# Kernel optimization log

Measured on AMD Instinct MI355X. Metric: run time of the kernel, lower is better.

The kernel has to match this reference:

```python
import jax, jax.numpy as jnp
import numpy as np

N = 100_000      # nodes
E = 1_600_000    # edges (avg degree 16)
F_IN = 128       # in_feats
H = 128          # n_hidden
H2 = 64          # n_hidden // 2


def setup_inputs() -> dict:
    key = jax.random.key(0)
    k1, k2, k3, k4, k5 = jax.random.split(key, 5)
    features = jax.random.normal(k1, (N, F_IN), dtype=jnp.float32)
    W1 = jax.random.normal(k2, (F_IN, H), dtype=jnp.float32) * 0.05
    W2 = jax.random.normal(k3, (H, H2), dtype=jnp.float32) * 0.05
    src = jax.random.randint(k4, (E,), 0, N, dtype=jnp.int32)
    dst = jax.random.randint(k5, (E,), 0, N, dtype=jnp.int32)
    return {"features": features, "W1": W1, "W2": W2, "src": src, "dst": dst}


def _graph_conv(h, W, src, dst, out_norm, in_norm):
    # DGL GraphConv, norm='both', bias=False:
    #   rst = D_dst^{-1/2} * (A @ (D_src^{-1/2} * h)) @ W
    # (weight applied before/after aggregation is mathematically identical)
    h = h * out_norm[:, None]                                   # scale source feats
    agg = jax.ops.segment_sum(h[src], dst, num_segments=N)      # SpMM: sum over in-edges
    return (agg * in_norm[:, None]) @ W


def reference(features, W1, W2, src, dst):
    ones = jnp.ones(src.shape[0], dtype=jnp.float32)
    # allow_zero_in_degree=True -> DGL clamps degrees to min 1 for norm
    out_deg = jnp.clip(jax.ops.segment_sum(ones, src, num_segments=N), 1.0)
    in_deg = jnp.clip(jax.ops.segment_sum(ones, dst, num_segments=N), 1.0)
    out_norm = out_deg ** -0.5
    in_norm = in_deg ** -0.5
    h = _graph_conv(features, W1, src, dst, out_norm, in_norm)  # [N, H]
    h = jax.nn.relu(h)
    return _graph_conv(h, W2, src, dst, out_norm, in_norm)      # [N, H2]
```

## Files before the change

kernel.cpp:

```cpp
#include <hip/hip_runtime.h>
#include <cstdint>
#include <cstddef>

#define NN 100000
#define NE 1600000
#define FD 128
#define HD2 64

#define BSH 7
#define BSZ 128
#define NB ((NN + BSZ - 1) / BSZ)
#define TILE 4096
#define NTILE ((NE + TILE - 1) / TILE)
#define CAPB 2560

static_assert(NB <= 1024, "single-block bucket scan assumes <=1024 buckets");

typedef short bf16x8_t __attribute__((ext_vector_type(8)));
typedef float f32x4_t __attribute__((ext_vector_type(4)));

static __device__ __forceinline__ uint f2bf(float x) {
  uint u = __float_as_uint(x);
  return (u + 0x7fffu + ((u >> 16) & 1u)) >> 16;
}
static __device__ __forceinline__ uint pack2(float lo, float hi) {
  return f2bf(lo) | (f2bf(hi) << 16);
}
static __device__ __forceinline__ float bflo(uint v) { return __uint_as_float(v << 16); }
static __device__ __forceinline__ float bfhi(uint v) { return __uint_as_float(v & 0xffff0000u); }

__global__ void k_bucket(const int* __restrict__ src, const int* __restrict__ dst,
                         int* __restrict__ bcnt_d, int* __restrict__ bcnt_s,
                         uint* __restrict__ brec_d, ushort* __restrict__ brec_s) {
  __shared__ int hd[NB], gbd[NB], hs[NB], gbs[NB];
  for (int i = threadIdx.x; i < NB; i += 256) { hd[i] = 0; hs[i] = 0; }
  __syncthreads();
  int base = blockIdx.x * TILE;
  for (int i = threadIdx.x; i < TILE; i += 256) {
    int e = base + i;
    if (e < NE) {
      atomicAdd(&hd[dst[e] >> BSH], 1);
      atomicAdd(&hs[src[e] >> BSH], 1);
    }
  }
  __syncthreads();
  for (int i = threadIdx.x; i < NB; i += 256) {
    int cd = hd[i], cs = hs[i];
    gbd[i] = cd ? atomicAdd(bcnt_d + i, cd) : 0;
    gbs[i] = cs ? atomicAdd(bcnt_s + i, cs) : 0;
    hd[i] = 0;
    hs[i] = 0;
  }
  __syncthreads();
  for (int i = threadIdx.x; i < TILE; i += 256) {
    int e = base + i;
    if (e < NE) {
      int d = dst[e], sv = src[e];
      int bd = d >> BSH, bs = sv >> BSH;
      int rd = gbd[bd] + atomicAdd(&hd[bd], 1);
      if (rd < CAPB)
        brec_d[(size_t)bd * CAPB + rd] = ((uint)(d & (BSZ - 1)) << 17) | (uint)sv;
      int rs = gbs[bs] + atomicAdd(&hs[bs], 1);
      if (rs < CAPB)
        brec_s[(size_t)bs * CAPB + rs] = (ushort)(sv & (BSZ - 1));
    }
  }
}

__global__ __launch_bounds__(1024) void k_bscan(const int* __restrict__ bcnt_d,
                                                int* __restrict__ boff_d) {
  __shared__ int s[1024];
  int t = threadIdx.x;
  int v = (t < NB) ? bcnt_d[t] : 0;
  s[t] = v;
  __syncthreads();
#pragma unroll
  for (int off = 1; off < 1024; off <<= 1) {
    int x = (t >= off) ? s[t - off] : 0;
    __syncthreads();
    s[t] += x;
    __syncthreads();
  }
  if (t < NB) boff_d[t + 1] = s[t];
  if (t == 0) boff_d[0] = 0;
}

__global__ __launch_bounds__(256) void k_build(const uint* __restrict__ brec_d,
                                               const ushort* __restrict__ brec_s,
                                               const int* __restrict__ bcnt_d,
                                               const int* __restrict__ bcnt_s,
                                               const int* __restrict__ boff,
                                               int* __restrict__ row_ptr,
                                               float* __restrict__ in_norm,
                                               float* __restrict__ out_norm,
                                               int* __restrict__ csr) {
  __shared__ int lcnt[BSZ];
  __shared__ int lscan[BSZ + 1];
  __shared__ int lcur[BSZ];
  __shared__ int lcsr[CAPB];
  const int t = threadIdx.x;
  const int b = blockIdx.x;
  const int d0 = b * BSZ;
  const int nd = min(BSZ, NN - d0);
  const size_t rbase = (size_t)b * CAPB;

  const int len = min(bcnt_d[b], CAPB);
  const int ebase = boff[b];
  for (int i = t; i < BSZ; i += 256) lcnt[i] = 0;
  __syncthreads();
  for (int e = t; e < len; e += 256)
    atomicAdd(&lcnt[brec_d[rbase + e] >> 17], 1);
  __syncthreads();
  for (int i = t; i < nd; i += 256)
    in_norm[d0 + i] = rsqrtf((float)max(lcnt[i], 1));

  if (t < BSZ) lcur[t] = lcnt[t];
  __syncthreads();
#pragma unroll
  for (int off = 1; off < BSZ; off <<= 1) {
    int x = (t >= off && t < BSZ) ? lcur[t - off] : 0;
    __syncthreads();
    if (t < BSZ) lcur[t] += x;
    __syncthreads();
  }
  if (t < BSZ) lscan[t + 1] = lcur[t];
  if (t == 0) lscan[0] = 0;
  __syncthreads();
  for (int i = t; i <= nd; i += 256) row_ptr[d0 + i] = ebase + lscan[i];
  if (t < BSZ) lcur[t] = lscan[t];
  __syncthreads();

  for (int e = t; e < len; e += 256) {
    uint r = brec_d[rbase + e];
    int p = atomicAdd(&lcur[r >> 17], 1);
    lcsr[p] = (int)(r & 0x1FFFFu);
  }
  __syncthreads();
  for (int ld = t; ld < nd; ld += 256) {
    int a = lscan[ld], bnd = lscan[ld + 1];
    for (int i = a + 1; i < bnd; ++i) {
      int v = lcsr[i];
      int j = i - 1;
      while (j >= a && lcsr[j] > v) { lcsr[j + 1] = lcsr[j]; --j; }
      lcsr[j + 1] = v;
    }
  }
  __syncthreads();
  for (int i = t; i < len; i += 256) csr[ebase + i] = lcsr[i];

  __syncthreads();
  for (int i = t; i < BSZ; i += 256) lcnt[i] = 0;
  __syncthreads();
  const int len_s = min(bcnt_s[b], CAPB);
  for (int e = t; e < len_s; e += 256)
    atomicAdd(&lcnt[brec_s[rbase + e]], 1);
  __syncthreads();
  for (int i = t; i < nd; i += 256)
    out_norm[d0 + i] = rsqrtf((float)max(lcnt[i], 1));
}

__global__ void k_prep(const float* __restrict__ feat, const float* __restrict__ onorm,
                       uint* __restrict__ Xb,
                       const float* __restrict__ W1, const float* __restrict__ W2,
                       uint* __restrict__ W1t, uint* __restrict__ W2t) {
  int t = blockIdx.x * 256 + threadIdx.x;
  if (t < NN * 64) {
    int row = t >> 6, j = t & 63;
    float2 f = *(const float2*)(feat + (size_t)row * FD + 2 * j);
    float w = onorm[row];
    Xb[t] = pack2(f.x * w, f.y * w);
  } else {
    int i = t - NN * 64;
    if (i < FD * 64) {
      int n = i >> 6, kk = i & 63;
      W1t[i] = pack2(W1[(size_t)(2 * kk) * FD + n], W1[(size_t)(2 * kk + 1) * FD + n]);
    } else {
      int i2 = i - FD * 64;
      int n = i2 >> 6, kk = i2 & 63;
      W2t[i2] = pack2(W2[(size_t)(2 * kk) * HD2 + n], W2[(size_t)(2 * kk + 1) * HD2 + n]);
    }
  }
}

__global__ void k_spmm1b(const uint* __restrict__ Xb, const int* __restrict__ row_ptr,
                         const int* __restrict__ csr_src, const float* __restrict__ in_norm,
                         uint* __restrict__ Hb1) {
  int gid = blockIdx.x * blockDim.x + threadIdx.x;
  int row = gid >> 6;
  if (row >= NN) return;
  int lane = threadIdx.x & 63;
  int grp = lane >> 4;
  int gl = lane & 15;
  int e0 = row_ptr[row], e1 = row_ptr[row + 1];
  float2 a0 = {0.f, 0.f}, a1 = {0.f, 0.f}, a2 = {0.f, 0.f}, a3 = {0.f, 0.f};
#define ACC1(v)                                  \
  a0.x += bflo((v).x); a0.y += bfhi((v).x);      \
  a1.x += bflo((v).y); a1.y += bfhi((v).y);      \
  a2.x += bflo((v).z); a2.y += bfhi((v).z);      \
  a3.x += bflo((v).w); a3.y += bfhi((v).w);
  int e = e0;
  for (; e + 16 <= e1; e += 16) {
    int s0 = csr_src[e + grp];
    int s1 = csr_src[e + 4 + grp];
    int s2 = csr_src[e + 8 + grp];
    int s3 = csr_src[e + 12 + grp];
    uint4 v0 = *(const uint4*)(Xb + ((size_t)s0 << 6) + (gl << 2));
    uint4 v1 = *(const uint4*)(Xb + ((size_t)s1 << 6) + (gl << 2));
    uint4 v2 = *(const uint4*)(Xb + ((size_t)s2 << 6) + (gl << 2));
    uint4 v3 = *(const uint4*)(Xb + ((size_t)s3 << 6) + (gl << 2));
    ACC1(v0);
    ACC1(v1);
    ACC1(v2);
    ACC1(v3);
  }
  for (; e + 4 <= e1; e += 4) {
    int s0 = csr_src[e + grp];
    uint4 v0 = *(const uint4*)(Xb + ((size_t)s0 << 6) + (gl << 2));
    ACC1(v0);
  }
  if (e + grp < e1) {
    int s0 = csr_src[e + grp];
    uint4 v0 = *(const uint4*)(Xb + ((size_t)s0 << 6) + (gl << 2));
    ACC1(v0);
  }
#undef ACC1
#pragma unroll
  for (int m = 16; m <= 32; m <<= 1) {
    a0.x += __shfl_xor(a0.x, m); a0.y += __shfl_xor(a0.y, m);
    a1.x += __shfl_xor(a1.x, m); a1.y += __shfl_xor(a1.y, m);
    a2.x += __shfl_xor(a2.x, m); a2.y += __shfl_xor(a2.y, m);
    a3.x += __shfl_xor(a3.x, m); a3.y += __shfl_xor(a3.y, m);
  }
  if (grp == 0) {
    float wi = in_norm[row];
    uint4 o;
    o.x = pack2(a0.x * wi, a0.y * wi);
    o.y = pack2(a1.x * wi, a1.y * wi);
    o.z = pack2(a2.x * wi, a2.y * wi);
    o.w = pack2(a3.x * wi, a3.y * wi);
    *(uint4*)(Hb1 + ((size_t)row << 6) + (gl << 2)) = o;
  }
}

__global__ __launch_bounds__(256) void k_mlp(const uint* __restrict__ Hb1,
                                             const uint* __restrict__ W1t,
                                             const uint* __restrict__ W2t,
                                             const float* __restrict__ onorm,
                                             ushort* __restrict__ Tb) {
  __shared__ ushort h_lds[64 * FD];
  char* const lds = (char*)h_lds;
  const int tid = threadIdx.x;
  const int wid = tid >> 6;
  const int lane = tid & 63;
  const int l15 = lane & 15;
  const int g = lane >> 4;
  const int rowbase = blockIdx.x * 64 + wid * 16;

  const int ar = min(rowbase + l15, NN - 1);
  const uint* Arow = Hb1 + (size_t)ar * 64;
  bf16x8_t afr[4];
#pragma unroll
  for (int kc = 0; kc < 4; ++kc)
    afr[kc] = *(const bf16x8_t*)(Arow + kc * 16 + g * 4);

  float wnorm[4];
#pragma unroll
  for (int r = 0; r < 4; ++r)
    wnorm[r] = onorm[min(rowbase + 4 * g + r, NN - 1)];

#pragma unroll
  for (int nf = 0; nf < 8; ++nf) {
    f32x4_t acc = {0.f, 0.f, 0.f, 0.f};
#pragma unroll
    for (int kc = 0; kc < 4; ++kc) {
      bf16x8_t b = *(const bf16x8_t*)(W1t + (size_t)(nf * 16 + l15) * 64 + kc * 16 + g * 4);
      acc = __builtin_amdgcn_mfma_f32_16x16x32_bf16(afr[kc], b, acc, 0, 0, 0);
    }
#pragma unroll
    for (int r = 0; r < 4; ++r) {
      float hv = fmaxf(acc[r], 0.f) * wnorm[r];
      int row = wid * 16 + 4 * g + r;
      int byte = row * 256 + (nf * 16 + l15) * 2;
      byte ^= (row & 7) << 4;
      *(ushort*)(lds + byte) = (ushort)f2bf(hv);
    }
  }
  __syncthreads();

  bf16x8_t a2[4];
#pragma unroll
  for (int kc = 0; kc < 4; ++kc) {
    int row = wid * 16 + l15;
    int byte = row * 256 + (kc * 32 + 8 * g) * 2;
    byte ^= (row & 7) << 4;
    a2[kc] = *(const bf16x8_t*)(lds + byte);
  }
#pragma unroll
  for (int nf = 0; nf < 4; ++nf) {
    f32x4_t acc = {0.f, 0.f, 0.f, 0.f};
#pragma unroll
    for (int kc = 0; kc < 4; ++kc) {
      bf16x8_t b = *(const bf16x8_t*)(W2t + (size_t)(nf * 16 + l15) * 64 + kc * 16 + g * 4);
      acc = __builtin_amdgcn_mfma_f32_16x16x32_bf16(a2[kc], b, acc, 0, 0, 0);
    }
#pragma unroll
    for (int r = 0; r < 4; ++r) {
      int row = rowbase + 4 * g + r;
      if (row < NN)
        Tb[(size_t)row * HD2 + nf * 16 + l15] = (ushort)f2bf(acc[r]);
    }
  }
}

__global__ void k_spmm2b(const uint* __restrict__ Tb, const int* __restrict__ row_ptr,
                         const int* __restrict__ csr_src, const float* __restrict__ in_norm,
                         float* __restrict__ out) {
  int gid = blockIdx.x * blockDim.x + threadIdx.x;
  int row = gid >> 6;
  if (row >= NN) return;
  int lane = threadIdx.x & 63;
  int grp = lane >> 4;
  int gl = lane & 15;
  int e0 = row_ptr[row], e1 = row_ptr[row + 1];
  float2 a0 = {0.f, 0.f}, a1 = {0.f, 0.f};
#define ACC2(v)                                  \
  a0.x += bflo((v).x); a0.y += bfhi((v).x);      \
  a1.x += bflo((v).y); a1.y += bfhi((v).y);
  int e = e0;
  for (; e + 16 <= e1; e += 16) {
    int s0 = csr_src[e + grp];
    int s1 = csr_src[e + 4 + grp];
    int s2 = csr_src[e + 8 + grp];
    int s3 = csr_src[e + 12 + grp];
    uint2 v0 = *(const uint2*)(Tb + ((size_t)s0 << 5) + (gl << 1));
    uint2 v1 = *(const uint2*)(Tb + ((size_t)s1 << 5) + (gl << 1));
    uint2 v2 = *(const uint2*)(Tb + ((size_t)s2 << 5) + (gl << 1));
    uint2 v3 = *(const uint2*)(Tb + ((size_t)s3 << 5) + (gl << 1));
    ACC2(v0);
    ACC2(v1);
    ACC2(v2);
    ACC2(v3);
  }
  for (; e + 4 <= e1; e += 4) {
    int s0 = csr_src[e + grp];
    uint2 v0 = *(const uint2*)(Tb + ((size_t)s0 << 5) + (gl << 1));
    ACC2(v0);
  }
  if (e + grp < e1) {
    int s0 = csr_src[e + grp];
    uint2 v0 = *(const uint2*)(Tb + ((size_t)s0 << 5) + (gl << 1));
    ACC2(v0);
  }
#undef ACC2
#pragma unroll
  for (int m = 16; m <= 32; m <<= 1) {
    a0.x += __shfl_xor(a0.x, m); a0.y += __shfl_xor(a0.y, m);
    a1.x += __shfl_xor(a1.x, m); a1.y += __shfl_xor(a1.y, m);
  }
  if (grp == 0) {
    float wi = in_norm[row];
    *(float4*)(out + (size_t)row * HD2 + gl * 4) =
        make_float4(a0.x * wi, a0.y * wi, a1.x * wi, a1.y * wi);
  }
}

extern "C" void kernel_launch(void* const* d_in, const int* in_sizes, int n_in,
                              void* d_out, int out_size, void* d_ws, size_t ws_size,
                              hipStream_t stream) {
  const float* feat = (const float*)d_in[0];
  const float* W1   = (const float*)d_in[1];
  const float* W2   = (const float*)d_in[2];
  const int*   src  = (const int*)d_in[3];
  const int*   dst  = (const int*)d_in[4];
  float* out = (float*)d_out;

  char* p = (char*)d_ws;
  auto take = [&p](size_t bytes) -> char* {
    char* r = p;
    p += (bytes + 511) & ~(size_t)511;
    return r;
  };
  int*   row_ptr  = (int*)take((size_t)(NN + 1) * 4);
  int*   bcnt     = (int*)take((size_t)2 * NB * 4);
  int*   boff_d   = (int*)take((size_t)(NB + 1) * 4);
  float* out_norm = (float*)take((size_t)NN * 4);
  float* in_norm  = (float*)take((size_t)NN * 4);
  int*   csr_src  = (int*)take((size_t)NE * 4);
  uint*  W1t      = (uint*)take((size_t)FD * 64 * 4);
  uint*  W2t      = (uint*)take((size_t)HD2 * 64 * 4);
  uint*  Xb       = (uint*)take((size_t)NN * 64 * 4);
  uint*  Hb1      = (uint*)take((size_t)NN * 64 * 4);
  int*   bcnt_d   = bcnt;
  int*   bcnt_s   = bcnt + NB;
  ushort* Tb      = (ushort*)Xb;
  uint*   brec_d  = (uint*)Hb1;
  ushort* brec_s  = (ushort*)(Hb1 + (size_t)NB * CAPB);

  hipMemsetAsync(bcnt, 0, (size_t)2 * NB * 4, stream);

  k_bucket<<<NTILE, 256, 0, stream>>>(src, dst, bcnt_d, bcnt_s, brec_d, brec_s);
  k_bscan <<<1, 1024, 0, stream>>>(bcnt_d, boff_d);
  k_build <<<NB, 256, 0, stream>>>(brec_d, brec_s, bcnt_d, bcnt_s, boff_d,
                                   row_ptr, in_norm, out_norm, csr_src);
  k_prep  <<<(NN * 64 + FD * 64 + HD2 * 64) / 256, 256, 0, stream>>>(feat, out_norm, Xb,
                                                                     W1, W2, W1t, W2t);

  k_spmm1b<<<(NN * 64) / 256, 256, 0, stream>>>(Xb, row_ptr, csr_src, in_norm, Hb1);
  k_mlp   <<<(NN + 63) / 64, 256, 0, stream>>>(Hb1, W1t, W2t, out_norm, Tb);
  k_spmm2b<<<(NN * 64) / 256, 256, 0, stream>>>((const uint*)Tb, row_ptr, csr_src, in_norm, out);
}
```

Measured before the change: 276.2 us.

## Fuse feature prep into bucketing kernel and pack source norm into CSR entries

The feature-to-bf16 conversion and weight transposes now run as extra blocks of the bucketing kernel, and out-degree norms are computed in a new kernel alongside the bucket scan. Because X is no longer pre-scaled by out_norm, k_build encodes a compressed out_norm value into the upper 15 bits of each CSR entry next to the 17-bit source index, and SpMM1 decodes it and applies it as an FMA weight. This removes a separate prep launch and its dependency on out_norm. In exchange, the norm is quantized to a truncated float, which adds small precision error, and the bucketing tile size is also doubled.

Result: faster. 266.7 us (-3.4%).

```diff
diff --git a/kernel.cpp b/kernel.cpp
--- a/kernel.cpp
+++ b/kernel.cpp
@@ -10,11 +10,12 @@
 #define BSH 7
 #define BSZ 128
 #define NB ((NN + BSZ - 1) / BSZ)
-#define TILE 4096
+#define TILE 8192
 #define NTILE ((NE + TILE - 1) / TILE)
 #define CAPB 2560
-
-static_assert(NB <= 1024, "single-block bucket scan assumes <=1024 buckets");
+#define NPREP ((NN * 64 + FD * 64 + HD2 * 64 + 255) / 256)
+
+static_assert(NB <= 1024, "bucket scan assumes <=1024 buckets");
 
 typedef short bf16x8_t __attribute__((ext_vector_type(8)));
 typedef float f32x4_t __attribute__((ext_vector_type(4)));
@@ -29,13 +30,39 @@
 static __device__ __forceinline__ float bflo(uint v) { return __uint_as_float(v << 16); }
 static __device__ __forceinline__ float bfhi(uint v) { return __uint_as_float(v & 0xffff0000u); }
 
-__global__ void k_bucket(const int* __restrict__ src, const int* __restrict__ dst,
-                         int* __restrict__ bcnt_d, int* __restrict__ bcnt_s,
-                         uint* __restrict__ brec_d, ushort* __restrict__ brec_s) {
+static __device__ __forceinline__ float dec_w(uint r) {
+  return __uint_as_float(((r >> 17) + 0x38000u) << 12);
+}
+
+__global__ void k_bucket_prep(const int* __restrict__ src, const int* __restrict__ dst,
+                              int* __restrict__ bcnt_d, int* __restrict__ bcnt_s,
+                              uint* __restrict__ brec_d, ushort* __restrict__ brec_s,
+                              const float* __restrict__ feat, uint* __restrict__ Xraw,
+                              const float* __restrict__ W1, const float* __restrict__ W2,
+                              uint* __restrict__ W1t, uint* __restrict__ W2t) {
   __shared__ int hd[NB], gbd[NB], hs[NB], gbs[NB];
+  const int bid = blockIdx.x;
+  if (bid >= NTILE) {
+    int i = (bid - NTILE) * 256 + threadIdx.x;
+    if (i < NN * 64) {
+      float2 f = *(const float2*)(feat + 2 * (size_t)i);
+      Xraw[i] = pack2(f.x, f.y);
+    } else {
+      int j = i - NN * 64;
+      if (j < FD * 64) {
+        int n = j >> 6, kk = j & 63;
+        W1t[j] = pack2(W1[(size_t)(2 * kk) * FD + n], W1[(size_t)(2 * kk + 1) * FD + n]);
+      } else if (j < FD * 64 + HD2 * 64) {
+        int j2 = j - FD * 64;
+        int n = j2 >> 6, kk = j2 & 63;
+        W2t[j2] = pack2(W2[(size_t)(2 * kk) * HD2 + n], W2[(size_t)(2 * kk + 1) * HD2 + n]);
+      }
+    }
+    return;
+  }
   for (int i = threadIdx.x; i < NB; i += 256) { hd[i] = 0; hs[i] = 0; }
   __syncthreads();
-  int base = blockIdx.x * TILE;
+  int base = bid * TILE;
   for (int i = threadIdx.x; i < TILE; i += 256) {
     int e = base + i;
     if (e < NE) {
@@ -67,33 +94,48 @@
   }
 }
 
-__global__ __launch_bounds__(1024) void k_bscan(const int* __restrict__ bcnt_d,
-                                                int* __restrict__ boff_d) {
-  __shared__ int s[1024];
-  int t = threadIdx.x;
-  int v = (t < NB) ? bcnt_d[t] : 0;
-  s[t] = v;
-  __syncthreads();
-#pragma unroll
-  for (int off = 1; off < 1024; off <<= 1) {
-    int x = (t >= off) ? s[t - off] : 0;
+__global__ __launch_bounds__(1024) void k_onorm_scan(const ushort* __restrict__ brec_s,
+                                                     const int* __restrict__ bcnt_s,
+                                                     float* __restrict__ out_norm,
+                                                     const int* __restrict__ bcnt_d,
+                                                     int* __restrict__ boff_d) {
+  __shared__ int sm[1024];
+  const int t = threadIdx.x;
+  const int b = blockIdx.x;
+  if (b < NB) {
+    if (t < BSZ) sm[t] = 0;
     __syncthreads();
-    s[t] += x;
+    const int len = min(bcnt_s[b], CAPB);
+    const size_t rbase = (size_t)b * CAPB;
+    for (int e = t; e < len; e += 1024)
+      atomicAdd(&sm[brec_s[rbase + e]], 1);
     __syncthreads();
-  }
-  if (t < NB) boff_d[t + 1] = s[t];
-  if (t == 0) boff_d[0] = 0;
+    const int s0 = b * BSZ;
+    const int ns = min(BSZ, NN - s0);
+    if (t < ns) out_norm[s0 + t] = rsqrtf((float)max(sm[t], 1));
+  } else {
+    int v = (t < NB) ? bcnt_d[t] : 0;
+    sm[t] = v;
+    __syncthreads();
+#pragma unroll
+    for (int off = 1; off < 1024; off <<= 1) {
+      int x = (t >= off) ? sm[t - off] : 0;
+      __syncthreads();
+      sm[t] += x;
+      __syncthreads();
+    }
+    if (t < NB) boff_d[t + 1] = sm[t];
+    if (t == 0) boff_d[0] = 0;
+  }
 }
 
 __global__ __launch_bounds__(256) void k_build(const uint* __restrict__ brec_d,
-                                               const ushort* __restrict__ brec_s,
                                                const int* __restrict__ bcnt_d,
-                                               const int* __restrict__ bcnt_s,
                                                const int* __restrict__ boff,
+                                               const float* __restrict__ onorm,
                                                int* __restrict__ row_ptr,
                                                float* __restrict__ in_norm,
-                                               float* __restrict__ out_norm,
-                                               int* __restrict__ csr) {
+                                               uint* __restrict__ csr) {
   __shared__ int lcnt[BSZ];
   __shared__ int lscan[BSZ + 1];
   __shared__ int lcur[BSZ];
@@ -103,9 +145,9 @@
   const int d0 = b * BSZ;
   const int nd = min(BSZ, NN - d0);
   const size_t rbase = (size_t)b * CAPB;
-
   const int len = min(bcnt_d[b], CAPB);
   const int ebase = boff[b];
+
   for (int i = t; i < BSZ; i += 256) lcnt[i] = 0;
   __syncthreads();
   for (int e = t; e < len; e += 256)
@@ -146,44 +188,15 @@
     }
   }
   __syncthreads();
-  for (int i = t; i < len; i += 256) csr[ebase + i] = lcsr[i];
-
-  __syncthreads();
-  for (int i = t; i < BSZ; i += 256) lcnt[i] = 0;
-  __syncthreads();
-  const int len_s = min(bcnt_s[b], CAPB);
-  for (int e = t; e < len_s; e += 256)
-    atomicAdd(&lcnt[brec_s[rbase + e]], 1);
-  __syncthreads();
-  for (int i = t; i < nd; i += 256)
-    out_norm[d0 + i] = rsqrtf((float)max(lcnt[i], 1));
-}
-
-__global__ void k_prep(const float* __restrict__ feat, const float* __restrict__ onorm,
-                       uint* __restrict__ Xb,
-                       const float* __restrict__ W1, const float* __restrict__ W2,
-                       uint* __restrict__ W1t, uint* __restrict__ W2t) {
-  int t = blockIdx.x * 256 + threadIdx.x;
-  if (t < NN * 64) {
-    int row = t >> 6, j = t & 63;
-    float2 f = *(const float2*)(feat + (size_t)row * FD + 2 * j);
-    float w = onorm[row];
-    Xb[t] = pack2(f.x * w, f.y * w);
-  } else {
-    int i = t - NN * 64;
-    if (i < FD * 64) {
-      int n = i >> 6, kk = i & 63;
-      W1t[i] = pack2(W1[(size_t)(2 * kk) * FD + n], W1[(size_t)(2 * kk + 1) * FD + n]);
-    } else {
-      int i2 = i - FD * 64;
-      int n = i2 >> 6, kk = i2 & 63;
-      W2t[i2] = pack2(W2[(size_t)(2 * kk) * HD2 + n], W2[(size_t)(2 * kk + 1) * HD2 + n]);
-    }
-  }
-}
-
-__global__ void k_spmm1b(const uint* __restrict__ Xb, const int* __restrict__ row_ptr,
-                         const int* __restrict__ csr_src, const float* __restrict__ in_norm,
+  for (int i = t; i < len; i += 256) {
+    int s = lcsr[i];
+    uint code = (__float_as_uint(onorm[s]) >> 12) - 0x38000u;
+    csr[ebase + i] = (code << 17) | (uint)s;
+  }
+}
+
+__global__ void k_spmm1b(const uint* __restrict__ Xraw, const int* __restrict__ row_ptr,
+                         const uint* __restrict__ csr, const float* __restrict__ in_norm,
                          uint* __restrict__ Hb1) {
   int gid = blockIdx.x * blockDim.x + threadIdx.x;
   int row = gid >> 6;
@@ -193,37 +206,40 @@
   int gl = lane & 15;
   int e0 = row_ptr[row], e1 = row_ptr[row + 1];
   float2 a0 = {0.f, 0.f}, a1 = {0.f, 0.f}, a2 = {0.f, 0.f}, a3 = {0.f, 0.f};
-#define ACC1(v)                                  \
-  a0.x += bflo((v).x); a0.y += bfhi((v).x);      \
-  a1.x += bflo((v).y); a1.y += bfhi((v).y);      \
-  a2.x += bflo((v).z); a2.y += bfhi((v).z);      \
-  a3.x += bflo((v).w); a3.y += bfhi((v).w);
+#define ACCW(v, ww)                                                       \
+  a0.x = fmaf(ww, bflo((v).x), a0.x); a0.y = fmaf(ww, bfhi((v).x), a0.y); \
+  a1.x = fmaf(ww, bflo((v).y), a1.x); a1.y = fmaf(ww, bfhi((v).y), a1.y); \
+  a2.x = fmaf(ww, bflo((v).z), a2.x); a2.y = fmaf(ww, bfhi((v).z), a2.y); \
+  a3.x = fmaf(ww, bflo((v).w), a3.x); a3.y = fmaf(ww, bfhi((v).w), a3.y);
   int e = e0;
   for (; e + 16 <= e1; e += 16) {
-    int s0 = csr_src[e + grp];
-    int s1 = csr_src[e + 4 + grp];
-    int s2 = csr_src[e + 8 + grp];
-    int s3 = csr_src[e + 12 + grp];
-    uint4 v0 = *(const uint4*)(Xb + ((size_t)s0 << 6) + (gl << 2));
-    uint4 v1 = *(const uint4*)(Xb + ((size_t)s1 << 6) + (gl << 2));
-    uint4 v2 = *(const uint4*)(Xb + ((size_t)s2 << 6) + (gl << 2));
-    uint4 v3 = *(const uint4*)(Xb + ((size_t)s3 << 6) + (gl << 2));
-    ACC1(v0);
-    ACC1(v1);
-    ACC1(v2);
-    ACC1(v3);
+    uint r0 = csr[e + grp];
+    uint r1 = csr[e + 4 + grp];
+    uint r2 = csr[e + 8 + grp];
+    uint r3 = csr[e + 12 + grp];
+    uint4 v0 = *(const uint4*)(Xraw + ((size_t)(r0 & 0x1FFFFu) << 6) + (gl << 2));
+    uint4 v1 = *(const uint4*)(Xraw + ((size_t)(r1 & 0x1FFFFu) << 6) + (gl << 2));
+    uint4 v2 = *(const uint4*)(Xraw + ((size_t)(r2 & 0x1FFFFu) << 6) + (gl << 2));
+    uint4 v3 = *(const uint4*)(Xraw + ((size_t)(r3 & 0x1FFFFu) << 6) + (gl << 2));
+    float w0 = dec_w(r0), w1 = dec_w(r1), w2 = dec_w(r2), w3 = dec_w(r3);
+    ACCW(v0, w0);
+    ACCW(v1, w1);
+    ACCW(v2, w2);
+    ACCW(v3, w3);
   }
   for (; e + 4 <= e1; e += 4) {
-    int s0 = csr_src[e + grp];
-    uint4 v0 = *(const uint4*)(Xb + ((size_t)s0 << 6) + (gl << 2));
-    ACC1(v0);
+    uint r0 = csr[e + grp];
+    uint4 v0 = *(const uint4*)(Xraw + ((size_t)(r0 & 0x1FFFFu) << 6) + (gl << 2));
+    float w0 = dec_w(r0);
+    ACCW(v0, w0);
   }
   if (e + grp < e1) {
-    int s0 = csr_src[e + grp];
-    uint4 v0 = *(const uint4*)(Xb + ((size_t)s0 << 6) + (gl << 2));
-    ACC1(v0);
-  }
-#undef ACC1
+    uint r0 = csr[e + grp];
+    uint4 v0 = *(const uint4*)(Xraw + ((size_t)(r0 & 0x1FFFFu) << 6) + (gl << 2));
+    float w0 = dec_w(r0);
+    ACCW(v0, w0);
+  }
+#undef ACCW
 #pragma unroll
   for (int m = 16; m <= 32; m <<= 1) {
     a0.x += __shfl_xor(a0.x, m); a0.y += __shfl_xor(a0.y, m);
@@ -313,7 +329,7 @@
 }
 
 __global__ void k_spmm2b(const uint* __restrict__ Tb, const int* __restrict__ row_ptr,
-                         const int* __restrict__ csr_src, const float* __restrict__ in_norm,
+                         const uint* __restrict__ csr, const float* __restrict__ in_norm,
                          float* __restrict__ out) {
   int gid = blockIdx.x * blockDim.x + threadIdx.x;
   int row = gid >> 6;
@@ -328,10 +344,10 @@
   a1.x += bflo((v).y); a1.y += bfhi((v).y);
   int e = e0;
   for (; e + 16 <= e1; e += 16) {
-    int s0 = csr_src[e + grp];
-    int s1 = csr_src[e + 4 + grp];
-    int s2 = csr_src[e + 8 + grp];
-    int s3 = csr_src[e + 12 + grp];
+    uint s0 = csr[e + grp] & 0x1FFFFu;
+    uint s1 = csr[e + 4 + grp] & 0x1FFFFu;
+    uint s2 = csr[e + 8 + grp] & 0x1FFFFu;
+    uint s3 = csr[e + 12 + grp] & 0x1FFFFu;
     uint2 v0 = *(const uint2*)(Tb + ((size_t)s0 << 5) + (gl << 1));
     uint2 v1 = *(const uint2*)(Tb + ((size_t)s1 << 5) + (gl << 1));
     uint2 v2 = *(const uint2*)(Tb + ((size_t)s2 << 5) + (gl << 1));
@@ -342,12 +358,12 @@
     ACC2(v3);
   }
   for (; e + 4 <= e1; e += 4) {
-    int s0 = csr_src[e + grp];
+    uint s0 = csr[e + grp] & 0x1FFFFu;
     uint2 v0 = *(const uint2*)(Tb + ((size_t)s0 << 5) + (gl << 1));
     ACC2(v0);
   }
   if (e + grp < e1) {
-    int s0 = csr_src[e + grp];
+    uint s0 = csr[e + grp] & 0x1FFFFu;
     uint2 v0 = *(const uint2*)(Tb + ((size_t)s0 << 5) + (gl << 1));
     ACC2(v0);
   }
@@ -385,27 +401,26 @@
   int*   boff_d   = (int*)take((size_t)(NB + 1) * 4);
   float* out_norm = (float*)take((size_t)NN * 4);
   float* in_norm  = (float*)take((size_t)NN * 4);
-  int*   csr_src  = (int*)take((size_t)NE * 4);
+  uint*  csr      = (uint*)take((size_t)NE * 4);
   uint*  W1t      = (uint*)take((size_t)FD * 64 * 4);
   uint*  W2t      = (uint*)take((size_t)HD2 * 64 * 4);
-  uint*  Xb       = (uint*)take((size_t)NN * 64 * 4);
+  uint*  Xraw     = (uint*)take((size_t)NN * 64 * 4);
   uint*  Hb1      = (uint*)take((size_t)NN * 64 * 4);
   int*   bcnt_d   = bcnt;
   int*   bcnt_s   = bcnt + NB;
-  ushort* Tb      = (ushort*)Xb;
+  ushort* Tb      = (ushort*)Xraw;
   uint*   brec_d  = (uint*)Hb1;
   ushort* brec_s  = (ushort*)(Hb1 + (size_t)NB * CAPB);
 
   hipMemsetAsync(bcnt, 0, (size_t)2 * NB * 4, stream);
 
-  k_bucket<<<NTILE, 256, 0, stream>>>(src, dst, bcnt_d, bcnt_s, brec_d, brec_s);
-  k_bscan <<<1, 1024, 0, stream>>>(bcnt_d, boff_d);
-  k_build <<<NB, 256, 0, stream>>>(brec_d, brec_s, bcnt_d, bcnt_s, boff_d,
-                                   row_ptr, in_norm, out_norm, csr_src);
-  k_prep  <<<(NN * 64 + FD * 64 + HD2 * 64) / 256, 256, 0, stream>>>(feat, out_norm, Xb,
-                                                                     W1, W2, W1t, W2t);
-
-  k_spmm1b<<<(NN * 64) / 256, 256, 0, stream>>>(Xb, row_ptr, csr_src, in_norm, Hb1);
+  k_bucket_prep<<<NTILE + NPREP, 256, 0, stream>>>(src, dst, bcnt_d, bcnt_s, brec_d, brec_s,
+                                                   feat, Xraw, W1, W2, W1t, W2t);
+  k_onorm_scan <<<NB + 1, 1024, 0, stream>>>(brec_s, bcnt_s, out_norm, bcnt_d, boff_d);
+  k_build      <<<NB, 256, 0, stream>>>(brec_d, bcnt_d, boff_d, out_norm,
+                                        row_ptr, in_norm, csr);
+
+  k_spmm1b<<<(NN * 64) / 256, 256, 0, stream>>>(Xraw, row_ptr, csr, in_norm, Hb1);
   k_mlp   <<<(NN + 63) / 64, 256, 0, stream>>>(Hb1, W1t, W2t, out_norm, Tb);
-  k_spmm2b<<<(NN * 64) / 256, 256, 0, stream>>>((const uint*)Tb, row_ptr, csr_src, in_norm, out);
-}
+  k_spmm2b<<<(NN * 64) / 256, 256, 0, stream>>>((const uint*)Tb, row_ptr, csr, in_norm, out);
+}
```
